# Kernel optimization log

Hardware: AMD Instinct MI355X
Metric: run time of the kernel (lower is better)

Reference implementation:

```python
import jax, jax.numpy as jnp
import numpy as np

B, C, H, W = 8, 256, 128, 128
SH, SW = 8, 8            # stoken_size
HH, WW = H // SH, W // SW
NH = 8                   # num_heads
HD = C // NH             # head_dim = 32
KD = HD                  # key_dim (attn_ratio=1)
ATTN_SCALE = KD ** (-0.5)
AFF_SCALE = C ** (-0.5)


def unfold9(x):
    """x: (B,C,hh,ww) -> (B, hh*ww, C, 9); matches Unfold(3) + transpose/reshape."""
    b, c, hh, ww = x.shape
    xp = jnp.pad(x, ((0, 0), (0, 0), (1, 1), (1, 1)))
    p = jnp.stack([xp[:, :, dy:dy + hh, dx:dx + ww]
                   for dy in range(3) for dx in range(3)], axis=2)  # (B,C,9,hh,ww)
    return p.transpose(0, 3, 4, 1, 2).reshape(b, hh * ww, c, 9)


def fold9(y):
    """y: (B,C,9,hh,ww) -> (B,C,hh,ww); matches Fold(3) (conv_transpose with identity kernels)."""
    hh, ww = y.shape[-2:]
    yp = jnp.pad(y, ((0, 0), (0, 0), (0, 0), (1, 1), (1, 1)))
    out = 0.
    for dy in range(3):
        for dx in range(3):
            out = out + yp[:, :, dy * 3 + dx, 2 - dy:2 - dy + hh, 2 - dx:2 - dx + ww]
    return out


def attention(sf, w_qkv, w_pe, w_proj):
    """Attention module with attn_ratio=1 (Conv layers have act=False, BN identity)."""
    b, c, hh, ww = sf.shape
    n = hh * ww
    qkv = jnp.einsum('oc,bchw->bohw', w_qkv, sf).reshape(b, NH, 2 * KD + HD, n)
    q, k, v = jnp.split(qkv, [KD, 2 * KD], axis=2)
    attn = jax.nn.softmax(jnp.einsum('bhkn,bhkm->bhnm', q, k) * ATTN_SCALE, axis=-1)
    o = jnp.einsum('bhdm,bhnm->bhdn', v, attn).reshape(b, c, hh, ww)
    pe = jax.lax.conv_general_dilated(
        v.reshape(b, c, hh, ww), w_pe, (1, 1), ((1, 1), (1, 1)),
        dimension_numbers=('NCHW', 'OIHW', 'NCHW'), feature_group_count=c)
    return jnp.einsum('oc,bchw->bohw', w_proj, o + pe)


def setup_inputs() -> dict:
    key = jax.random.key(0)
    k0, k1, k2, k3 = jax.random.split(key, 4)
    x = jax.random.normal(k0, (B, C, H, W), dtype=jnp.float32)
    w_qkv = jax.random.normal(k1, (3 * C, C), dtype=jnp.float32) * 0.05
    w_pe = jax.random.normal(k2, (C, 1, 3, 3), dtype=jnp.float32) * 0.05
    w_proj = jax.random.normal(k3, (C, C), dtype=jnp.float32) * 0.05
    return {'x': x, 'w_qkv': w_qkv, 'w_pe': w_pe, 'w_proj': w_proj}


def reference(x, w_qkv, w_pe, w_proj):
    # H,W divisible by stoken_size -> no padding branch
    xb = x.reshape(B, C, HH, SH, WW, SW)
    stoken = xb.mean(axis=(3, 5))                                   # (B,C,hh,ww) adaptive_avg_pool2d
    pix = xb.transpose(0, 2, 4, 3, 5, 1).reshape(B, HH * WW, SH * SW, C)
    # --- single no-grad iteration (n_iter=1) ---
    sf9 = unfold9(stoken)                                            # (B,n,C,9)
    aff = jax.nn.softmax(jnp.einsum('bnpc,bnck->bnpk', pix, sf9) * AFF_SCALE, axis=-1)
    aff = jax.lax.stop_gradient(aff)                                 # torch.no_grad
    asum = aff.sum(axis=2).transpose(0, 2, 1).reshape(B, 1, 9, HH, WW)
    asum = jax.lax.stop_gradient(fold9(asum))                        # (B,1,hh,ww)
    # --- super-token aggregation ---
    sf = jnp.einsum('bnpc,bnpk->bnck', pix, aff)                     # (B,n,C,9)
    sf = fold9(sf.transpose(0, 2, 3, 1).reshape(B, C, 9, HH, WW))    # (B,C,hh,ww)
    sf = sf / (asum + 1e-12)
    # --- refine with attention ---
    sf = attention(sf, w_qkv, w_pe, w_proj)
    # --- scatter back to pixels ---
    sf9b = unfold9(sf)                                               # (B,n,C,9)
    pix_out = jnp.einsum('bnck,bnpk->bnpc', sf9b, aff)               # (B,n,h*w,C)
    return pix_out.reshape(B, HH, WW, C, SH, SW).transpose(0, 3, 1, 4, 2, 5).reshape(B, C, H, W)
```

## Files before the change

### kernel.cpp

```cpp
#include <hip/hip_runtime.h>
#include <cstdint>
#include <cstddef>


#define AFF_SCALE 0.0625f
#define ATTN_SCALE 0.17677669529663687f

__global__ __launch_bounds__(128) void stoken_kernel(
    const float* __restrict__ x, float* __restrict__ stok_pad)
{
    int blk = blockIdx.x;
    int i  = blk & 15;
    int bc = blk >> 4;
    int t  = threadIdx.x;
    const float* xr = x + ((size_t)bc * 128 + i * 8) * 128 + t;
    float s = 0.f;
#pragma unroll
    for (int r = 0; r < 8; ++r) s += xr[r * 128];
    s += __shfl_down(s, 4, 64);
    s += __shfl_down(s, 2, 64);
    s += __shfl_down(s, 1, 64);
    if ((t & 7) == 0) {
        int j = t >> 3;
        stok_pad[((size_t)bc * 18 + (i + 1)) * 18 + (j + 1)] = s * (1.f / 64.f);
    }
}

__global__ __launch_bounds__(256) void aff_agg_kernel(
    const float* __restrict__ x, const float* __restrict__ stok_pad,
    float* __restrict__ aff_g, float* __restrict__ asum_g,
    float* __restrict__ agg)
{
    __shared__ __align__(16) float pixs[256 * 68];
    __shared__ __align__(16) float sfs[9 * 260];
    __shared__ __align__(16) float part[64 * 9];

    int bid  = blockIdx.x;
    int xcd  = bid & 7, slot = bid >> 3;
    int pair = xcd * 128 + (slot >> 1);
    int m = pair & 7, i = (pair >> 3) & 15, b = pair >> 7;
    int j = m * 2 + (slot & 1);
    int bn = b * 256 + i * 16 + j;
    int t = threadIdx.x;

    {
        int c0 = t >> 3, pi = t & 7;
#pragma unroll
        for (int it = 0; it < 8; ++it) {
            int c = c0 + 32 * it;
            const float* xp = x + (((size_t)b * 256 + c) * 128 + i * 8 + pi) * 128 + j * 8;
            float4 f0 = *(const float4*)&xp[0];
            float4 f1 = *(const float4*)&xp[4];
            *(float4*)&pixs[c * 68 + pi * 8]     = f0;
            *(float4*)&pixs[c * 68 + pi * 8 + 4] = f1;
        }
    }
    {
        const float* sp = stok_pad + ((size_t)b * 256 + t) * 324 + i * 18 + j;
#pragma unroll
        for (int dy = 0; dy < 3; ++dy)
#pragma unroll
            for (int dx = 0; dx < 3; ++dx)
                sfs[(dy * 3 + dx) * 260 + t] = sp[dy * 18 + dx];
    }
    part[t] = 0.f;
    part[t + 256] = 0.f;
    if (t < 64) part[t + 512] = 0.f;
    __syncthreads();

    {
        int s = t >> 6, p = t & 63;
        float acc[9] = {0.f,0.f,0.f,0.f,0.f,0.f,0.f,0.f,0.f};
        int cb = s * 64;
        for (int c4 = 0; c4 < 64; c4 += 4) {
            int c = cb + c4;
            float px0 = pixs[(c + 0) * 68 + p];
            float px1 = pixs[(c + 1) * 68 + p];
            float px2 = pixs[(c + 2) * 68 + p];
            float px3 = pixs[(c + 3) * 68 + p];
#pragma unroll
            for (int k = 0; k < 9; ++k) {
                const float4 sv = *(const float4*)&sfs[k * 260 + c];
                acc[k] += px0 * sv.x + px1 * sv.y + px2 * sv.z + px3 * sv.w;
            }
        }
#pragma unroll
        for (int k = 0; k < 9; ++k) atomicAdd(&part[p * 9 + k], acc[k]);
    }
    __syncthreads();

    float* affs = sfs;

    if (t < 64) {
        float a[9];
        float mx = -1e30f;
#pragma unroll
        for (int k = 0; k < 9; ++k) {
            float v = part[t * 9 + k] * AFF_SCALE;
            a[k] = v;
            mx = fmaxf(mx, v);
        }
        float ssum = 0.f;
#pragma unroll
        for (int k = 0; k < 9; ++k) { a[k] = __expf(a[k] - mx); ssum += a[k]; }
        float inv = 1.f / ssum;
#pragma unroll
        for (int k = 0; k < 9; ++k) {
            a[k] *= inv;
            affs[k * 64 + t] = a[k];
            aff_g[(size_t)bn * 576 + k * 64 + t] = a[k];
        }
#pragma unroll
        for (int k = 0; k < 9; ++k) {
            float r = a[k];
            r += __shfl_down(r, 32, 64); r += __shfl_down(r, 16, 64);
            r += __shfl_down(r, 8, 64);  r += __shfl_down(r, 4, 64);
            r += __shfl_down(r, 2, 64);  r += __shfl_down(r, 1, 64);
            if (t == 0) asum_g[(size_t)bn * 9 + k] = r;
        }
    }
    __syncthreads();

    {
        int c = t;
        int rot = (c >> 3) & 15;
        float a9[9] = {0.f,0.f,0.f,0.f,0.f,0.f,0.f,0.f,0.f};
        for (int p4i = 0; p4i < 16; ++p4i) {
            int p4 = (p4i + rot) & 15;
            const float4 pv = *(const float4*)&pixs[c * 68 + p4 * 4];
#pragma unroll
            for (int k = 0; k < 9; ++k) {
                const float4 av = *(const float4*)&affs[k * 64 + p4 * 4];
                a9[k] += pv.x * av.x + pv.y * av.y + pv.z * av.z + pv.w * av.w;
            }
        }
#pragma unroll
        for (int k = 0; k < 9; ++k)
            agg[((size_t)bn * 9 + k) * 256 + c] = a9[k];
    }
}

__global__ __launch_bounds__(256) void fold_div_kernel(
    const float* __restrict__ agg, const float* __restrict__ asum_g,
    float* __restrict__ sf)
{
    __shared__ float v[256 * 17];
    int b = blockIdx.x >> 4, y = blockIdx.x & 15;
    int t = threadIdx.x;
    for (int x = 0; x < 16; ++x) {
        float af = 0.f, val = 0.f;
#pragma unroll
        for (int dy = 0; dy < 3; ++dy)
#pragma unroll
            for (int dx = 0; dx < 3; ++dx) {
                int ii = y + 1 - dy, jj = x + 1 - dx;
                if ((unsigned)ii < 16u && (unsigned)jj < 16u) {
                    int idx = (b * 256 + ii * 16 + jj) * 9 + dy * 3 + dx;
                    af  += asum_g[idx];
                    val += agg[(size_t)idx * 256 + t];
                }
            }
        v[t * 17 + x] = val / (af + 1e-12f);
    }
    __syncthreads();
    int xw = t & 15, cw0 = t >> 4;
#pragma unroll
    for (int it = 0; it < 16; ++it) {
        int c = cw0 + it * 16;
        sf[((size_t)b * 256 + c) * 256 + y * 16 + xw] = v[c * 17 + xw];
    }
}

__global__ __launch_bounds__(256) void gemm_w(
    const float* __restrict__ A, const float* __restrict__ Bm,
    float* __restrict__ Cout, int M, int mode)
{
    __shared__ float As[32 * 68];
    __shared__ float Bs[32 * 64];
    int b = blockIdx.x, o0 = blockIdx.y * 64, n0 = blockIdx.z * 64;
    int t = threadIdx.x;
    int tr = t >> 4, tc = t & 15;
    const float* Bb = Bm + (size_t)b * 256 * 256;
    float acc[4][4];
#pragma unroll
    for (int ii = 0; ii < 4; ++ii)
#pragma unroll
        for (int jj = 0; jj < 4; ++jj) acc[ii][jj] = 0.f;

    for (int k0 = 0; k0 < 256; k0 += 32) {
        {
            int ol = t >> 2, kq = (t & 3) * 8;
            const float* Ap = A + (size_t)(o0 + ol) * 256 + k0 + kq;
            const float4 f0 = *(const float4*)&Ap[0];
            const float4 f1 = *(const float4*)&Ap[4];
            As[(kq + 0) * 68 + ol] = f0.x; As[(kq + 1) * 68 + ol] = f0.y;
            As[(kq + 2) * 68 + ol] = f0.z; As[(kq + 3) * 68 + ol] = f0.w;
            As[(kq + 4) * 68 + ol] = f1.x; As[(kq + 5) * 68 + ol] = f1.y;
            As[(kq + 6) * 68 + ol] = f1.z; As[(kq + 7) * 68 + ol] = f1.w;
        }
#pragma unroll
        for (int i2 = 0; i2 < 8; ++i2) {
            int e = t + i2 * 256;
            int kl = e >> 6, nl = e & 63;
            Bs[kl * 64 + nl] = Bb[(size_t)(k0 + kl) * 256 + n0 + nl];
        }
        __syncthreads();
#pragma unroll
        for (int kk = 0; kk < 32; ++kk) {
            const float4 av = *(const float4*)&As[kk * 68 + tr * 4];
            const float4 bv = *(const float4*)&Bs[kk * 64 + tc * 4];
            acc[0][0] += av.x * bv.x; acc[0][1] += av.x * bv.y; acc[0][2] += av.x * bv.z; acc[0][3] += av.x * bv.w;
            acc[1][0] += av.y * bv.x; acc[1][1] += av.y * bv.y; acc[1][2] += av.y * bv.z; acc[1][3] += av.y * bv.w;
            acc[2][0] += av.z * bv.x; acc[2][1] += av.z * bv.y; acc[2][2] += av.z * bv.z; acc[2][3] += av.z * bv.w;
            acc[3][0] += av.w * bv.x; acc[3][1] += av.w * bv.y; acc[3][2] += av.w * bv.z; acc[3][3] += av.w * bv.w;
        }
        __syncthreads();
    }

    if (mode == 0) {
#pragma unroll
        for (int ii = 0; ii < 4; ++ii) {
            int o = o0 + tr * 4 + ii;
            float4 st = make_float4(acc[ii][0], acc[ii][1], acc[ii][2], acc[ii][3]);
            *(float4*)&Cout[((size_t)b * M + o) * 256 + n0 + tc * 4] = st;
        }
    } else {
#pragma unroll
        for (int jj = 0; jj < 4; ++jj) {
            int n = n0 + tc * 4 + jj;
            int y = n >> 4, x = n & 15;
            float4 st = make_float4(acc[0][jj], acc[1][jj], acc[2][jj], acc[3][jj]);
            *(float4*)&Cout[(((size_t)b * 18 + 1 + y) * 18 + 1 + x) * 256 + o0 + tr * 4] = st;
        }
    }
}

__global__ __launch_bounds__(256) void attn_kernel(
    const float* __restrict__ qkv, float* __restrict__ o_attn)
{
    __shared__ float smem[9216];
    int b = blockIdx.x, h = blockIdx.y, nt = blockIdx.z;
    int t = threadIdx.x, nl = t & 63, mq = t >> 6;
    int n = nt * 64 + nl;

    {
        int dd = t >> 3, mb = (t & 7) * 32;
        const float* krow = qkv + ((size_t)b * 768 + h * 96 + 32 + dd) * 256;
#pragma unroll
        for (int e4 = 0; e4 < 8; ++e4) {
            int m = mb + e4 * 4;
            const float4 kw = *(const float4*)&krow[m];
            smem[(m + 0) * 32 + dd] = kw.x; smem[(m + 1) * 32 + dd] = kw.y;
            smem[(m + 2) * 32 + dd] = kw.z; smem[(m + 3) * 32 + dd] = kw.w;
        }
    }
    float q[32];
    {
        const float* qbase = qkv + ((size_t)b * 768 + h * 96) * 256 + n;
#pragma unroll
        for (int d = 0; d < 32; ++d) q[d] = qbase[(size_t)d * 256];
    }
    __syncthreads();

    float l[64];
#pragma unroll
    for (int e = 0; e < 64; ++e) {
        const float* kp = &smem[(mq * 64 + e) * 32];
        float s = 0.f;
#pragma unroll
        for (int d4 = 0; d4 < 8; ++d4) {
            const float4 kv4 = *(const float4*)&kp[d4 * 4];
            s += q[d4 * 4 + 0] * kv4.x + q[d4 * 4 + 1] * kv4.y +
                 q[d4 * 4 + 2] * kv4.z + q[d4 * 4 + 3] * kv4.w;
        }
        l[e] = s * ATTN_SCALE;
    }
    float mx = -1e30f;
#pragma unroll
    for (int e = 0; e < 64; ++e) mx = fmaxf(mx, l[e]);
    float sm = 0.f;
#pragma unroll
    for (int e = 0; e < 64; ++e) { l[e] = __expf(l[e] - mx); sm += l[e]; }
    __syncthreads();

    {
        int dd = t >> 3, mb = (t & 7) * 32;
        const float* vrow = qkv + ((size_t)b * 768 + h * 96 + 64 + dd) * 256;
#pragma unroll
        for (int e4 = 0; e4 < 8; ++e4) {
            int m = mb + e4 * 4;
            const float4 vw = *(const float4*)&vrow[m];
            smem[(m + 0) * 32 + dd] = vw.x; smem[(m + 1) * 32 + dd] = vw.y;
            smem[(m + 2) * 32 + dd] = vw.z; smem[(m + 3) * 32 + dd] = vw.w;
        }
    }
    __syncthreads();

    float oa[32];
#pragma unroll
    for (int d = 0; d < 32; ++d) oa[d] = 0.f;
#pragma unroll
    for (int e = 0; e < 64; ++e) {
        float pm = l[e];
        const float* vp = &smem[(mq * 64 + e) * 32];
#pragma unroll
        for (int d4 = 0; d4 < 8; ++d4) {
            const float4 vv = *(const float4*)&vp[d4 * 4];
            oa[d4 * 4 + 0] += pm * vv.x; oa[d4 * 4 + 1] += pm * vv.y;
            oa[d4 * 4 + 2] += pm * vv.z; oa[d4 * 4 + 3] += pm * vv.w;
        }
    }
    __syncthreads();

    float* op   = smem;
    float* mxsm = smem + 8448;
    {
        int idx = mq * 64 + nl;
#pragma unroll
        for (int d = 0; d < 32; ++d) op[idx * 33 + d] = oa[d];
        mxsm[idx * 2 + 0] = mx;
        mxsm[idx * 2 + 1] = sm;
    }
    __syncthreads();

    if (t < 64) {
        float M2 = -1e30f;
#pragma unroll
        for (int q4 = 0; q4 < 4; ++q4) M2 = fmaxf(M2, mxsm[(q4 * 64 + t) * 2]);
        float w[4], S = 0.f;
#pragma unroll
        for (int q4 = 0; q4 < 4; ++q4) {
            w[q4] = __expf(mxsm[(q4 * 64 + t) * 2] - M2);
            S += mxsm[(q4 * 64 + t) * 2 + 1] * w[q4];
        }
        float inv = 1.f / S;
#pragma unroll
        for (int d = 0; d < 32; ++d) {
            float o = 0.f;
#pragma unroll
            for (int q4 = 0; q4 < 4; ++q4) o += op[(q4 * 64 + t) * 33 + d] * w[q4];
            o_attn[((size_t)b * 256 + h * 32 + d) * 256 + nt * 64 + t] = o * inv;
        }
    }
}

__global__ __launch_bounds__(256) void peadd_kernel(
    const float* __restrict__ qkv, const float* __restrict__ w_pe,
    float* __restrict__ o_attn)
{
    int bc = blockIdx.x;
    int b = bc >> 8, c = bc & 255;
    int t = threadIdx.x;
    int y = t >> 4, x = t & 15;
    int h = c >> 5, d = c & 31;
    const float* v = qkv + ((size_t)b * 768 + h * 96 + 64 + d) * 256;
    float acc = o_attn[(size_t)bc * 256 + t];
#pragma unroll
    for (int ky = 0; ky < 3; ++ky)
#pragma unroll
        for (int kx = 0; kx < 3; ++kx) {
            int yy = y + ky - 1, xx = x + kx - 1;
            if ((unsigned)yy < 16u && (unsigned)xx < 16u)
                acc += w_pe[c * 9 + ky * 3 + kx] * v[yy * 16 + xx];
        }
    o_attn[(size_t)bc * 256 + t] = acc;
}

__global__ __launch_bounds__(256) void scatter_kernel(
    const float* __restrict__ sfa_pad, const float* __restrict__ aff_g,
    float* __restrict__ out)
{
    __shared__ float ss[3 * 18 * 40];
    __shared__ float aff_s[16 * 577];

    int blk = blockIdx.x;
    int pi = blk & 7, i = (blk >> 3) & 15, b = blk >> 7;
    int t = threadIdx.x;

    for (int e = t; e < 1728; e += 256) {
        int dy = e / 576, rem = e % 576;
        int col = rem >> 5, idx = rem & 31;
        int q = idx >> 3, d = idx & 7;
        ss[(dy * 18 + col) * 40 + idx] =
            sfa_pad[(((size_t)b * 18 + i + dy) * 18 + col) * 256 + q * 64 + pi * 8 + d];
    }
    {
        const float* ag = aff_g + ((size_t)b * 256 + i * 16) * 576;
        for (int e = t; e < 9216; e += 256) {
            int j = e / 576, rem = e % 576;
            int k = rem >> 6, p = rem & 63;
            aff_s[j * 577 + p * 9 + k] = ag[j * 576 + rem];
        }
    }
    __syncthreads();

    int lane = t & 63, w = t >> 6;
    int j0 = lane >> 3, pj = lane & 7;
    int j1 = j0 + 8;

    float S0[4][9], S1[4][9];
#pragma unroll
    for (int q = 0; q < 4; ++q)
#pragma unroll
        for (int k = 0; k < 9; ++k) {
            int dy = k / 3, dx = k % 3;
            S0[q][k] = ss[(dy * 18 + j0 + dx) * 40 + q * 8 + pj];
            S1[q][k] = ss[(dy * 18 + j1 + dx) * 40 + q * 8 + pj];
        }

    int y = i * 8 + pi;
    size_t ob = (size_t)b * 256 * 16384 + (size_t)y * 128;
    const float* A0 = &aff_s[j0 * 577];
    const float* A1 = &aff_s[j1 * 577];
    for (int p = w * 16; p < w * 16 + 16; ++p) {
        float a0[9], a1[9];
#pragma unroll
        for (int k = 0; k < 9; ++k) { a0[k] = A0[p * 9 + k]; a1[k] = A1[p * 9 + k]; }
#pragma unroll
        for (int q = 0; q < 4; ++q) {
            int c2 = p * 4 + q;
            float v0 = 0.f, v1 = 0.f;
#pragma unroll
            for (int k = 0; k < 9; ++k) {
                v0 += S0[q][k] * a0[k];
                v1 += S1[q][k] * a1[k];
            }
            out[ob + (size_t)c2 * 16384 + lane] = v0;
            out[ob + (size_t)c2 * 16384 + 64 + lane] = v1;
        }
    }
}

extern "C" void kernel_launch(void* const* d_in, const int* in_sizes, int n_in,
                              void* d_out, int out_size, void* d_ws, size_t ws_size,
                              hipStream_t stream) {
    const float* x      = (const float*)d_in[0];
    const float* w_qkv  = (const float*)d_in[1];
    const float* w_pe   = (const float*)d_in[2];
    const float* w_proj = (const float*)d_in[3];
    float* out = (float*)d_out;
    float* agg = (float*)d_out;

    float* ws = (float*)d_ws;
    const size_t o_aff  = 0;
    const size_t o_asum = 1179648;
    const size_t o_pad  = 1198080;
    const size_t o_sf   = 1861632;
    const size_t o_qkv  = 2385920;

    hipMemsetAsync(ws + o_pad, 0, 663552 * sizeof(float), stream);

    stoken_kernel<<<8 * 256 * 16, 128, 0, stream>>>(x, ws + o_pad);
    aff_agg_kernel<<<8 * 256, 256, 0, stream>>>(x, ws + o_pad, ws + o_aff,
                                                ws + o_asum, agg);
    fold_div_kernel<<<8 * 16, 256, 0, stream>>>(agg, ws + o_asum, ws + o_sf);
    gemm_w<<<dim3(8, 12, 4), 256, 0, stream>>>(w_qkv, ws + o_sf, ws + o_qkv, 768, 0);
    hipMemsetAsync(ws + o_pad, 0, 663552 * sizeof(float), stream);
    attn_kernel<<<dim3(8, 8, 4), 256, 0, stream>>>(ws + o_qkv, ws + o_sf);
    peadd_kernel<<<8 * 256, 256, 0, stream>>>(ws + o_qkv, w_pe, ws + o_sf);
    gemm_w<<<dim3(8, 4, 4), 256, 0, stream>>>(w_proj, ws + o_sf, ws + o_pad, 256, 1);
    scatter_kernel<<<8 * 16 * 8, 256, 0, stream>>>(ws + o_pad, ws + o_aff, out);
}
```

Before: 447.3 us.

## Register-tile affinity GEMMs in aff_agg, swizzle pixel smem, make stoken channel-last

The padded super-token buffer is switched to channel-last layout, so the 3x3 neighbourhood gather in aff_agg_kernel reads contiguous channels across threads. Both small GEMMs in aff_agg_kernel (pixel·super-token affinity, and the pixel·affinity aggregation) are rewritten so each thread computes a 4x9 register tile from float4 LDS reads. The partial sums are reduced with xor shuffles instead of scalar loads. Pixel tiles in shared memory get an XOR swizzle to avoid bank conflicts under the new access pattern. This costs more registers and shuffle instructions and may lower occupancy.

```diff
diff --git a/kernel.cpp b/kernel.cpp
--- a/kernel.cpp
+++ b/kernel.cpp
@@ -22,7 +22,9 @@
     s += __shfl_down(s, 1, 64);
     if ((t & 7) == 0) {
         int j = t >> 3;
-        stok_pad[((size_t)bc * 18 + (i + 1)) * 18 + (j + 1)] = s * (1.f / 64.f);
+        int b = bc >> 8, c = bc & 255;
+        stok_pad[(((size_t)b * 18 + (i + 1)) * 18 + (j + 1)) * 256 + c] =
+            s * (1.f / 64.f);
     }
 }
 
@@ -33,13 +35,13 @@
 {
     __shared__ __align__(16) float pixs[256 * 68];
     __shared__ __align__(16) float sfs[9 * 260];
-    __shared__ __align__(16) float part[64 * 9];
+    __shared__ __align__(16) float part[576];
 
     int bid  = blockIdx.x;
-    int xcd  = bid & 7, slot = bid >> 3;
-    int pair = xcd * 128 + (slot >> 1);
+    int xcd  = bid & 7, slot_ = bid >> 3;
+    int pair = xcd * 128 + (slot_ >> 1);
     int m = pair & 7, i = (pair >> 3) & 15, b = pair >> 7;
-    int j = m * 2 + (slot & 1);
+    int j = m * 2 + (slot_ & 1);
     int bn = b * 256 + i * 16 + j;
     int t = threadIdx.x;
 
@@ -51,41 +53,68 @@
             const float* xp = x + (((size_t)b * 256 + c) * 128 + i * 8 + pi) * 128 + j * 8;
             float4 f0 = *(const float4*)&xp[0];
             float4 f1 = *(const float4*)&xp[4];
-            *(float4*)&pixs[c * 68 + pi * 8]     = f0;
-            *(float4*)&pixs[c * 68 + pi * 8 + 4] = f1;
-        }
-    }
-    {
-        const float* sp = stok_pad + ((size_t)b * 256 + t) * 324 + i * 18 + j;
+            int gma = (c >> 2) & 3;
+            int s0 = (2 * pi) ^ gma, s1 = (2 * pi + 1) ^ gma;
+            *(float4*)&pixs[c * 68 + s0 * 4] = f0;
+            *(float4*)&pixs[c * 68 + s1 * 4] = f1;
+        }
+    }
+    {
+        const float* spT = stok_pad + (size_t)b * 324 * 256;
 #pragma unroll
         for (int dy = 0; dy < 3; ++dy)
 #pragma unroll
             for (int dx = 0; dx < 3; ++dx)
-                sfs[(dy * 3 + dx) * 260 + t] = sp[dy * 18 + dx];
+                sfs[(dy * 3 + dx) * 260 + t] =
+                    spT[((size_t)(i + dy) * 18 + (j + dx)) * 256 + t];
     }
     part[t] = 0.f;
     part[t + 256] = 0.f;
     if (t < 64) part[t + 512] = 0.f;
     __syncthreads();
 
-    {
-        int s = t >> 6, p = t & 63;
-        float acc[9] = {0.f,0.f,0.f,0.f,0.f,0.f,0.f,0.f,0.f};
-        int cb = s * 64;
-        for (int c4 = 0; c4 < 64; c4 += 4) {
-            int c = cb + c4;
-            float px0 = pixs[(c + 0) * 68 + p];
-            float px1 = pixs[(c + 1) * 68 + p];
-            float px2 = pixs[(c + 2) * 68 + p];
-            float px3 = pixs[(c + 3) * 68 + p];
+    int w = t >> 6, l = t & 63;
+
+    {
+        int pq = l >> 2, cgl = l & 3;
+        int cbase = w * 64 + cgl * 16;
+        float acc[4][9];
+#pragma unroll
+        for (int ii = 0; ii < 4; ++ii)
+#pragma unroll
+            for (int k = 0; k < 9; ++k) acc[ii][k] = 0.f;
+
+#pragma unroll
+        for (int c4i = 0; c4i < 4; ++c4i) {
+            int c = cbase + c4i * 4;
+            int slot = (pq ^ c4i) * 4;
+            const float4 p0 = *(const float4*)&pixs[(c + 0) * 68 + slot];
+            const float4 p1 = *(const float4*)&pixs[(c + 1) * 68 + slot];
+            const float4 p2 = *(const float4*)&pixs[(c + 2) * 68 + slot];
+            const float4 p3 = *(const float4*)&pixs[(c + 3) * 68 + slot];
 #pragma unroll
             for (int k = 0; k < 9; ++k) {
                 const float4 sv = *(const float4*)&sfs[k * 260 + c];
-                acc[k] += px0 * sv.x + px1 * sv.y + px2 * sv.z + px3 * sv.w;
+                acc[0][k] += p0.x * sv.x + p1.x * sv.y + p2.x * sv.z + p3.x * sv.w;
+                acc[1][k] += p0.y * sv.x + p1.y * sv.y + p2.y * sv.z + p3.y * sv.w;
+                acc[2][k] += p0.z * sv.x + p1.z * sv.y + p2.z * sv.z + p3.z * sv.w;
+                acc[3][k] += p0.w * sv.x + p1.w * sv.y + p2.w * sv.z + p3.w * sv.w;
             }
         }
 #pragma unroll
-        for (int k = 0; k < 9; ++k) atomicAdd(&part[p * 9 + k], acc[k]);
+        for (int ii = 0; ii < 4; ++ii)
+#pragma unroll
+            for (int k = 0; k < 9; ++k) {
+                acc[ii][k] += __shfl_xor(acc[ii][k], 1, 64);
+                acc[ii][k] += __shfl_xor(acc[ii][k], 2, 64);
+            }
+#pragma unroll
+        for (int k = 0; k < 9; ++k) {
+            float v01 = (cgl & 1) ? acc[1][k] : acc[0][k];
+            float v23 = (cgl & 1) ? acc[3][k] : acc[2][k];
+            float vk  = (cgl & 2) ? v23 : v01;
+            atomicAdd(&part[l * 9 + k], vk);
+        }
     }
     __syncthreads();
 
@@ -122,21 +151,47 @@
     __syncthreads();
 
     {
-        int c = t;
-        int rot = (c >> 3) & 15;
-        float a9[9] = {0.f,0.f,0.f,0.f,0.f,0.f,0.f,0.f,0.f};
-        for (int p4i = 0; p4i < 16; ++p4i) {
-            int p4 = (p4i + rot) & 15;
-            const float4 pv = *(const float4*)&pixs[c * 68 + p4 * 4];
+        int cql = l >> 2, pq2 = l & 3;
+        int cb2 = w * 64 + cql * 4;
+        int gma = cql & 3;
+        float acc2[4][9];
+#pragma unroll
+        for (int ii = 0; ii < 4; ++ii)
+#pragma unroll
+            for (int k = 0; k < 9; ++k) acc2[ii][k] = 0.f;
+
+#pragma unroll
+        for (int pp = 0; pp < 4; ++pp) {
+            int p4 = pq2 * 4 + pp;
+            int slot = (p4 ^ gma) * 4;
+            const float4 q0 = *(const float4*)&pixs[(cb2 + 0) * 68 + slot];
+            const float4 q1 = *(const float4*)&pixs[(cb2 + 1) * 68 + slot];
+            const float4 q2 = *(const float4*)&pixs[(cb2 + 2) * 68 + slot];
+            const float4 q3 = *(const float4*)&pixs[(cb2 + 3) * 68 + slot];
 #pragma unroll
             for (int k = 0; k < 9; ++k) {
                 const float4 av = *(const float4*)&affs[k * 64 + p4 * 4];
-                a9[k] += pv.x * av.x + pv.y * av.y + pv.z * av.z + pv.w * av.w;
+                acc2[0][k] += q0.x * av.x + q0.y * av.y + q0.z * av.z + q0.w * av.w;
+                acc2[1][k] += q1.x * av.x + q1.y * av.y + q1.z * av.z + q1.w * av.w;
+                acc2[2][k] += q2.x * av.x + q2.y * av.y + q2.z * av.z + q2.w * av.w;
+                acc2[3][k] += q3.x * av.x + q3.y * av.y + q3.z * av.z + q3.w * av.w;
             }
         }
 #pragma unroll
-        for (int k = 0; k < 9; ++k)
-            agg[((size_t)bn * 9 + k) * 256 + c] = a9[k];
+        for (int ii = 0; ii < 4; ++ii)
+#pragma unroll
+            for (int k = 0; k < 9; ++k) {
+                acc2[ii][k] += __shfl_xor(acc2[ii][k], 1, 64);
+                acc2[ii][k] += __shfl_xor(acc2[ii][k], 2, 64);
+            }
+        int cout = w * 64 + l;
+#pragma unroll
+        for (int k = 0; k < 9; ++k) {
+            float v01 = (pq2 & 1) ? acc2[1][k] : acc2[0][k];
+            float v23 = (pq2 & 1) ? acc2[3][k] : acc2[2][k];
+            float vk  = (pq2 & 2) ? v23 : v01;
+            agg[((size_t)bn * 9 + k) * 256 + cout] = vk;
+        }
     }
 }
 
```

After: 442.9 us. About the same (-1.0%).
